# Optimization experiments

Hardware: AMD Instinct MI355X
Metric: run time of the kernel (lower is better)

The kernel has to match this reference:

```python
import jax, jax.numpy as jnp
import numpy as np

BATCH = 1024
SEQ = 80
VOCAB = 50000
EMB = 512
UNITS = 512


def setup_inputs() -> dict:
    key = jax.random.key(0)
    ks = jax.random.split(key, 10)
    s_in = 1.0 / np.sqrt(EMB)
    s_h = 1.0 / np.sqrt(UNITS)
    return {
        "inputs": jax.random.randint(ks[0], (BATCH, SEQ), 0, VOCAB, dtype=jnp.int64),
        "emb": jax.random.normal(ks[1], (VOCAB, EMB), dtype=jnp.float32) * 0.05,
        "W0x": jax.random.normal(ks[2], (EMB, UNITS), dtype=jnp.float32) * s_in,
        "W0h": jax.random.normal(ks[3], (UNITS, UNITS), dtype=jnp.float32) * s_h,
        "b0": jnp.zeros((UNITS,), dtype=jnp.float32),
        "W1x": jax.random.normal(ks[4], (UNITS, UNITS), dtype=jnp.float32) * s_h,
        "W1h": jax.random.normal(ks[5], (UNITS, UNITS), dtype=jnp.float32) * s_h,
        "b1": jnp.zeros((UNITS,), dtype=jnp.float32),
        "Wout": jax.random.normal(ks[6], (UNITS, 1), dtype=jnp.float32) * s_h,
        "bout": jnp.zeros((1,), dtype=jnp.float32),
    }


def reference(inputs, emb, W0x, W0h, b0, W1x, W1h, b1, Wout, bout):
    # Embedding lookup: [B, T, E]
    x = emb[inputs]
    # Time-major for scan: [T, B, E]
    xs = jnp.transpose(x, (1, 0, 2))

    h0 = jnp.zeros((inputs.shape[0], W0h.shape[0]), dtype=emb.dtype)
    h1 = jnp.zeros((inputs.shape[0], W1h.shape[0]), dtype=emb.dtype)

    def step(carry, x_t):
        h0, h1 = carry
        # SimpleRNNCell 0: tanh(x@Wx + h@Wh + b)  (dropout inactive at inference)
        h0 = jnp.tanh(x_t @ W0x + h0 @ W0h + b0)
        # SimpleRNNCell 1 stacked on cell 0's output
        h1 = jnp.tanh(h0 @ W1x + h1 @ W1h + b1)
        return (h0, h1), None

    (h0, h1), _ = jax.lax.scan(step, (h0, h1), xs)
    # Dense(1) on last-step hidden of layer 1, then sigmoid -> [B, 1]
    prob = jax.nn.sigmoid(h1 @ Wout + bout)
    return prob
```

## Files before the change

### kernel.cpp

```cpp
#include <hip/hip_runtime.h>
#include <hip/hip_bf16.h>
#include <math.h>

#define BATCH   1024
#define SEQ     80
#define EMB     512
#define UNITS   512
#define NBG     16
#define NJ      8
#define THREADS 512

#define H0_OFF (2u * 1024 * 1024)
#define H1_OFF (4u * 1024 * 1024)
#define FL_OFF (6u * 1024 * 1024)

typedef __attribute__((ext_vector_type(8))) short              bf16x8;
typedef __attribute__((ext_vector_type(8))) unsigned short     u16x8;
typedef __attribute__((ext_vector_type(4))) float              f32x4;
typedef __attribute__((ext_vector_type(2))) unsigned long long u64x2;

__device__ inline unsigned short f2bf(float f) {
    __hip_bfloat16 h = __float2bfloat16(f);
    return *reinterpret_cast<unsigned short*>(&h);
}
__device__ inline float bf2f(unsigned short u) {
    unsigned int x = ((unsigned int)u) << 16;
    return __uint_as_float(x);
}
__device__ inline float tanh_fast(float x) {
    float e = __expf(2.f * x);
    return 1.f - 2.f / (e + 1.f);
}
__device__ inline u16x8 pack8(float4 p0, float4 p1) {
    u16x8 v;
    v[0]=f2bf(p0.x); v[1]=f2bf(p0.y); v[2]=f2bf(p0.z); v[3]=f2bf(p0.w);
    v[4]=f2bf(p1.x); v[5]=f2bf(p1.y); v[6]=f2bf(p1.z); v[7]=f2bf(p1.w);
    return v;
}
__device__ inline void st_u16(unsigned short* p, unsigned short v) {
    __hip_atomic_store(p, v, __ATOMIC_RELAXED, __HIP_MEMORY_SCOPE_AGENT);
}
__device__ inline unsigned long long ld_u64(const unsigned long long* p) {
    return __hip_atomic_load(p, __ATOMIC_RELAXED, __HIP_MEMORY_SCOPE_AGENT);
}
__device__ inline int ld_flag(const int* p) {
    return __hip_atomic_load(p, __ATOMIC_RELAXED, __HIP_MEMORY_SCOPE_AGENT);
}

__global__ __launch_bounds__(256) void pack_weights(
    const float* __restrict__ W0x, const float* __restrict__ W0h,
    const float* __restrict__ W1x, const float* __restrict__ W1h,
    unsigned short* __restrict__ wpack)
{
    int g    = blockIdx.x * 4 + (threadIdx.x >> 6);
    int lane = threadIdx.x & 63;
    int type = g >> 10;
    int j    = (g >> 7) & 7;
    int mat  = (g >> 6) & 1;
    int kk   = (g >> 2) & 15;
    int nt   = g & 3;
    const float* M = type ? (mat ? W1h : W1x) : (mat ? W0h : W0x);
    int col  = j * 64 + nt * 16 + (lane & 15);
    int rowb = kk * 32 + (lane >> 4) * 8;

    u16x8 v;
#pragma unroll
    for (int jj = 0; jj < 8; ++jj)
        v[jj] = f2bf(M[(size_t)(rowb + jj) * UNITS + col]);
    *(u16x8*)(wpack + (size_t)g * 512 + lane * 8) = v;
}

#define WLD(mat, kk, nt)            ((((mat)*16 + (kk))*4 + (nt)) * 512)
#define RNG(slot, kkl, row, quad)   (((((slot)*2 + (kkl))*64 + (row))*4 + (quad)) * 8)

#define GATHER_GEMM(HB, PAR, MAT, A0, A1)                                      \
    do {                                                                       \
        const unsigned long long* hs_ = (const unsigned long long*)            \
            ((HB) + ((size_t)(PAR) * BATCH + rbase) * UNITS);                  \
        const int go_ = grow * 128 + gk8 * 2;                                  \
        u64x2 ld_[8];                                                          \
        _Pragma("unroll")                                                      \
        for (int s_ = 0; s_ < 3; ++s_) {                                       \
            ld_[s_][0] = ld_u64(hs_ + go_ + s_ * 16);                          \
            ld_[s_][1] = ld_u64(hs_ + go_ + s_ * 16 + 1);                      \
        }                                                                      \
        _Pragma("unroll")                                                      \
        for (int s_ = 0; s_ < 8; ++s_) {                                       \
            *(u64x2*)(ring + RNG(s_ & 1, gk8 >> 2, grow, gk8 & 3)) = ld_[s_];  \
            __syncthreads();                                                   \
            if (s_ + 3 < 8) {                                                  \
                ld_[s_+3][0] = ld_u64(hs_ + go_ + (s_+3) * 16);                \
                ld_[s_+3][1] = ld_u64(hs_ + go_ + (s_+3) * 16 + 1);            \
            }                                                                  \
            _Pragma("unroll")                                                  \
            for (int kl_ = 0; kl_ < 2; ++kl_) {                                \
                bf16x8 a_ = *(const bf16x8*)(ring + RNG(s_ & 1, kl_, arow, quad)); \
                int kg_ = s_ * 2 + kl_;                                        \
                A0 = __builtin_amdgcn_mfma_f32_16x16x32_bf16(a_,               \
                    *(const bf16x8*)(wlds + WLD(MAT, kg_, nt0) + lane*8), A0, 0,0,0); \
                A1 = __builtin_amdgcn_mfma_f32_16x16x32_bf16(a_,               \
                    *(const bf16x8*)(wlds + WLD(MAT, kg_, nt1) + lane*8), A1, 0,0,0); \
            }                                                                  \
        }                                                                      \
    } while (0)

#define XSTAGE_GEMM(TT, A0, A1)                                                \
    do {                                                                       \
        int t_   = (TT) < SEQ ? (TT) : SEQ - 1;                                \
        int idx_ = inputs[(rbase + grow) * SEQ + t_];                          \
        const float4* ep_ = (const float4*)(emb + (size_t)idx_ * EMB) + gk8*2; \
        float4 pa_[8], pb_[8];                                                 \
        _Pragma("unroll")                                                      \
        for (int s_ = 0; s_ < 3; ++s_) { pa_[s_] = ep_[s_*16]; pb_[s_] = ep_[s_*16+1]; } \
        _Pragma("unroll")                                                      \
        for (int s_ = 0; s_ < 8; ++s_) {                                       \
            *(u16x8*)(ring + RNG(s_ & 1, gk8 >> 2, grow, gk8 & 3)) =           \
                pack8(pa_[s_], pb_[s_]);                                       \
            __syncthreads();                                                   \
            if (s_ + 3 < 8) { pa_[s_+3] = ep_[(s_+3)*16]; pb_[s_+3] = ep_[(s_+3)*16+1]; } \
            _Pragma("unroll")                                                  \
            for (int kl_ = 0; kl_ < 2; ++kl_) {                                \
                bf16x8 a_ = *(const bf16x8*)(ring + RNG(s_ & 1, kl_, arow, quad)); \
                int kg_ = s_ * 2 + kl_;                                        \
                A0 = __builtin_amdgcn_mfma_f32_16x16x32_bf16(a_,               \
                    *(const bf16x8*)(wlds + WLD(0, kg_, nt0) + lane*8), A0, 0,0,0); \
                A1 = __builtin_amdgcn_mfma_f32_16x16x32_bf16(a_,               \
                    *(const bf16x8*)(wlds + WLD(0, kg_, nt1) + lane*8), A1, 0,0,0); \
            }                                                                  \
        }                                                                      \
    } while (0)

#define PUBLISH(HB, PAR, A0, A1)                                               \
    do {                                                                       \
        unsigned short* d_ = (HB) +                                            \
            ((size_t)(PAR) * BATCH + rbase + rg * 16 + quad * 4) * UNITS       \
            + c0 + l15;                                                        \
        _Pragma("unroll")                                                      \
        for (int i_ = 0; i_ < 4; ++i_) {                                       \
            st_u16(d_ + (size_t)i_ * UNITS + nt0 * 16, f2bf(tanh_fast(A0[i_]))); \
            st_u16(d_ + (size_t)i_ * UNITS + nt1 * 16, f2bf(tanh_fast(A1[i_]))); \
        }                                                                      \
    } while (0)

__global__ __launch_bounds__(THREADS, 1) void rnn_ls(
    const int*   __restrict__ inputs,
    const float* __restrict__ emb,
    const float* __restrict__ b0,
    const float* __restrict__ b1,
    const unsigned short* __restrict__ wpack,
    unsigned short* __restrict__ h0buf,
    unsigned short* __restrict__ h1buf,
    int* __restrict__ flag0,
    int* __restrict__ flag1,
    const float* __restrict__ Wout,
    const float* __restrict__ bout,
    float*       __restrict__ out)
{
    __shared__ __align__(16) unsigned short wlds[2 * 16 * 4 * 512];
    __shared__ __align__(16) unsigned short ring[2 * 2 * 64 * 4 * 8];

    const int tid   = threadIdx.x;
    const int w     = tid >> 6;
    const int lane  = tid & 63;
    const int quad  = lane >> 4;
    const int l15   = lane & 15;
    const int type  = blockIdx.x >> 7;
    const int bidx  = blockIdx.x & 127;
    const int bg    = bidx >> 3;
    const int j     = bidx & 7;
    const int rbase = bg * 64;
    const int c0    = j * 64;

    const int rg   = w >> 1;
    const int ntp  = w & 1;
    const int nt0  = 2 * ntp, nt1 = nt0 + 1;
    const int arow = rg * 16 + l15;
    const int grow = tid >> 3;
    const int gk8  = tid & 7;

    {
        const unsigned short* wsrc = wpack + (size_t)(type * 8 + j) * 128 * 512;
#pragma unroll
        for (int i = 0; i < 16; ++i)
            *(u16x8*)(wlds + (size_t)(i * 512 + tid) * 8) =
                *(const u16x8*)(wsrc + (size_t)(i * 512 + tid) * 8);
    }
    __syncthreads();

    const float* bp   = type ? b1 : b0;
    const float  bia0 = bp[c0 + nt0 * 16 + l15];
    const float  bia1 = bp[c0 + nt1 * 16 + l15];

    if (type == 0) {
        f32x4 aX0 = {bia0, bia0, bia0, bia0};
        f32x4 aX1 = {bia1, bia1, bia1, bia1};
        XSTAGE_GEMM(0, aX0, aX1);

        for (int r = 0; r < SEQ; ++r) {
            const int par = r & 1;
            if (tid < 8)
                while (ld_flag(flag0 + bg * 8 + tid) < r)
                    __builtin_amdgcn_s_sleep(1);
            else if (tid < 16)
                while (ld_flag(flag1 + bg * 8 + (tid - 8)) < r - 1)
                    __builtin_amdgcn_s_sleep(1);
            __asm__ volatile("" ::: "memory");
            __syncthreads();

            f32x4 a0 = aX0, a1 = aX1;
            GATHER_GEMM(h0buf, par ^ 1, 1, a0, a1);
            PUBLISH(h0buf, par, a0, a1);
            __syncthreads();
            if (tid == 0)
                __hip_atomic_store(flag0 + bg * 8 + j, r + 1,
                                   __ATOMIC_RELEASE, __HIP_MEMORY_SCOPE_AGENT);

            aX0 = (f32x4){bia0, bia0, bia0, bia0};
            aX1 = (f32x4){bia1, bia1, bia1, bia1};
            XSTAGE_GEMM(r + 1, aX0, aX1);
        }
    } else {
        for (int s = 0; s < SEQ; ++s) {
            const int par = s & 1;
            if (tid < 8)
                while (ld_flag(flag0 + bg * 8 + tid) < s + 1)
                    __builtin_amdgcn_s_sleep(1);
            else if (tid < 16)
                while (ld_flag(flag1 + bg * 8 + (tid - 8)) < s)
                    __builtin_amdgcn_s_sleep(1);
            __asm__ volatile("" ::: "memory");
            __syncthreads();

            f32x4 a0 = {bia0, bia0, bia0, bia0};
            f32x4 a1 = {bia1, bia1, bia1, bia1};
            GATHER_GEMM(h0buf, par,     0, a0, a1);
            GATHER_GEMM(h1buf, par ^ 1, 1, a0, a1);
            PUBLISH(h1buf, par, a0, a1);
            __syncthreads();
            if (tid == 0)
                __hip_atomic_store(flag1 + bg * 8 + j, s + 1,
                                   __ATOMIC_RELEASE, __HIP_MEMORY_SCOPE_AGENT);
        }

        if (j == 0) {
            if (tid < 8)
                while (ld_flag(flag1 + bg * 8 + tid) < SEQ)
                    __builtin_amdgcn_s_sleep(1);
            __asm__ volatile("" ::: "memory");
            __syncthreads();
            const unsigned long long* hs = (const unsigned long long*)
                (h1buf + ((size_t)((SEQ - 1) & 1) * BATCH + rbase) * UNITS);
#pragma unroll
            for (int i = 0; i < 8; ++i) {
                int row = w * 8 + i;
                unsigned long long q0 = ld_u64(hs + row * 128 + lane * 2);
                unsigned long long q1 = ld_u64(hs + row * 128 + lane * 2 + 1);
                u64x2 qq; qq[0] = q0; qq[1] = q1;
                u16x8 hv = *(u16x8*)&qq;
                float sacc = 0.f;
#pragma unroll
                for (int k = 0; k < 8; ++k)
                    sacc += bf2f(hv[k]) * Wout[lane * 8 + k];
#pragma unroll
                for (int off = 32; off > 0; off >>= 1)
                    sacc += __shfl_down(sacc, off);
                if (lane == 0) {
                    float z = sacc + bout[0];
                    out[rbase + row] = 1.f / (1.f + __expf(-z));
                }
            }
        }
    }
}

extern "C" void kernel_launch(void* const* d_in, const int* in_sizes, int n_in,
                              void* d_out, int out_size, void* d_ws, size_t ws_size,
                              hipStream_t stream) {
    const int*   inputs = (const int*)d_in[0];
    const float* emb    = (const float*)d_in[1];
    const float* W0x    = (const float*)d_in[2];
    const float* W0h    = (const float*)d_in[3];
    const float* b0     = (const float*)d_in[4];
    const float* W1x    = (const float*)d_in[5];
    const float* W1h    = (const float*)d_in[6];
    const float* b1     = (const float*)d_in[7];
    const float* Wout   = (const float*)d_in[8];
    const float* bout   = (const float*)d_in[9];
    float*       out    = (float*)d_out;

    unsigned short* wpack = (unsigned short*)d_ws;
    unsigned short* h0buf = (unsigned short*)((char*)d_ws + H0_OFF);
    unsigned short* h1buf = (unsigned short*)((char*)d_ws + H1_OFF);
    int* flag0 = (int*)((char*)d_ws + FL_OFF);
    int* flag1 = flag0 + 128;

    hipMemsetAsync((char*)d_ws + FL_OFF, 0, 1024, stream);
    hipMemsetAsync((char*)h0buf + (size_t)BATCH * UNITS * 2, 0,
                   (size_t)BATCH * UNITS * 2, stream);
    hipMemsetAsync((char*)h1buf + (size_t)BATCH * UNITS * 2, 0,
                   (size_t)BATCH * UNITS * 2, stream);
    pack_weights<<<512, 256, 0, stream>>>(W0x, W0h, W1x, W1h, wpack);
    rnn_ls<<<256, THREADS, 0, stream>>>(
        inputs, emb, b0, b1, wpack, h0buf, h1buf, flag0, flag1,
        Wout, bout, out);
}
```

Measured before the change: 1.277 ms.

## Load RNN activations directly into registers instead of staging through LDS ring

Replaces the cooperative LDS ring buffer (with per-slice __syncthreads) for hidden-state and embedding tiles with per-lane direct global loads of MFMA A-fragments into registers, then runs all 16 k-steps back to back. This removes the many barriers and LDS round trips inside every recurrent step. In exchange each wave loads its own rows redundantly and holds up to 32 bf16x8 fragments in registers. Launch bounds are also changed to allow two blocks per CU, which tightens the register budget.

```diff
diff --git a/kernel.cpp b/kernel.cpp
--- a/kernel.cpp
+++ b/kernel.cpp
@@ -70,64 +70,48 @@
     *(u16x8*)(wpack + (size_t)g * 512 + lane * 8) = v;
 }
 
-#define WLD(mat, kk, nt)            ((((mat)*16 + (kk))*4 + (nt)) * 512)
-#define RNG(slot, kkl, row, quad)   (((((slot)*2 + (kkl))*64 + (row))*4 + (quad)) * 8)
-
-#define GATHER_GEMM(HB, PAR, MAT, A0, A1)                                      \
+#define WLD(mat, kk, nt)  ((((mat)*16 + (kk))*4 + (nt)) * 512)
+
+#define GATHER_REG(AV, HB, PAR)                                                \
     do {                                                                       \
         const unsigned long long* hs_ = (const unsigned long long*)            \
-            ((HB) + ((size_t)(PAR) * BATCH + rbase) * UNITS);                  \
-        const int go_ = grow * 128 + gk8 * 2;                                  \
-        u64x2 ld_[8];                                                          \
-        _Pragma("unroll")                                                      \
-        for (int s_ = 0; s_ < 3; ++s_) {                                       \
-            ld_[s_][0] = ld_u64(hs_ + go_ + s_ * 16);                          \
-            ld_[s_][1] = ld_u64(hs_ + go_ + s_ * 16 + 1);                      \
-        }                                                                      \
-        _Pragma("unroll")                                                      \
-        for (int s_ = 0; s_ < 8; ++s_) {                                       \
-            *(u64x2*)(ring + RNG(s_ & 1, gk8 >> 2, grow, gk8 & 3)) = ld_[s_];  \
-            __syncthreads();                                                   \
-            if (s_ + 3 < 8) {                                                  \
-                ld_[s_+3][0] = ld_u64(hs_ + go_ + (s_+3) * 16);                \
-                ld_[s_+3][1] = ld_u64(hs_ + go_ + (s_+3) * 16 + 1);            \
-            }                                                                  \
-            _Pragma("unroll")                                                  \
-            for (int kl_ = 0; kl_ < 2; ++kl_) {                                \
-                bf16x8 a_ = *(const bf16x8*)(ring + RNG(s_ & 1, kl_, arow, quad)); \
-                int kg_ = s_ * 2 + kl_;                                        \
-                A0 = __builtin_amdgcn_mfma_f32_16x16x32_bf16(a_,               \
-                    *(const bf16x8*)(wlds + WLD(MAT, kg_, nt0) + lane*8), A0, 0,0,0); \
-                A1 = __builtin_amdgcn_mfma_f32_16x16x32_bf16(a_,               \
-                    *(const bf16x8*)(wlds + WLD(MAT, kg_, nt1) + lane*8), A1, 0,0,0); \
-            }                                                                  \
-        }                                                                      \
-    } while (0)
-
-#define XSTAGE_GEMM(TT, A0, A1)                                                \
+            ((HB) + ((size_t)(PAR) * BATCH + rbase + arow) * UNITS);           \
+        _Pragma("unroll")                                                      \
+        for (int ks_ = 0; ks_ < 16; ++ks_) {                                   \
+            u64x2 q_;                                                          \
+            q_[0] = ld_u64(hs_ + ks_ * 8 + quad * 2);                          \
+            q_[1] = ld_u64(hs_ + ks_ * 8 + quad * 2 + 1);                      \
+            (AV)[ks_] = *(bf16x8*)&q_;                                         \
+        }                                                                      \
+    } while (0)
+
+#define GEMM_LDS(AV, MAT, A0, A1)                                              \
+    do {                                                                       \
+        _Pragma("unroll")                                                      \
+        for (int kg_ = 0; kg_ < 16; ++kg_) {                                   \
+            bf16x8 b0_ = *(const bf16x8*)(wlds + WLD(MAT, kg_, nt0) + lane*8); \
+            bf16x8 b1_ = *(const bf16x8*)(wlds + WLD(MAT, kg_, nt1) + lane*8); \
+            A0 = __builtin_amdgcn_mfma_f32_16x16x32_bf16((AV)[kg_], b0_, A0,   \
+                                                         0, 0, 0);             \
+            A1 = __builtin_amdgcn_mfma_f32_16x16x32_bf16((AV)[kg_], b1_, A1,   \
+                                                         0, 0, 0);             \
+        }                                                                      \
+    } while (0)
+
+#define XSTAGE_REG(TT, A0, A1)                                                 \
     do {                                                                       \
         int t_   = (TT) < SEQ ? (TT) : SEQ - 1;                                \
-        int idx_ = inputs[(rbase + grow) * SEQ + t_];                          \
-        const float4* ep_ = (const float4*)(emb + (size_t)idx_ * EMB) + gk8*2; \
-        float4 pa_[8], pb_[8];                                                 \
-        _Pragma("unroll")                                                      \
-        for (int s_ = 0; s_ < 3; ++s_) { pa_[s_] = ep_[s_*16]; pb_[s_] = ep_[s_*16+1]; } \
-        _Pragma("unroll")                                                      \
-        for (int s_ = 0; s_ < 8; ++s_) {                                       \
-            *(u16x8*)(ring + RNG(s_ & 1, gk8 >> 2, grow, gk8 & 3)) =           \
-                pack8(pa_[s_], pb_[s_]);                                       \
-            __syncthreads();                                                   \
-            if (s_ + 3 < 8) { pa_[s_+3] = ep_[(s_+3)*16]; pb_[s_+3] = ep_[(s_+3)*16+1]; } \
-            _Pragma("unroll")                                                  \
-            for (int kl_ = 0; kl_ < 2; ++kl_) {                                \
-                bf16x8 a_ = *(const bf16x8*)(ring + RNG(s_ & 1, kl_, arow, quad)); \
-                int kg_ = s_ * 2 + kl_;                                        \
-                A0 = __builtin_amdgcn_mfma_f32_16x16x32_bf16(a_,               \
-                    *(const bf16x8*)(wlds + WLD(0, kg_, nt0) + lane*8), A0, 0,0,0); \
-                A1 = __builtin_amdgcn_mfma_f32_16x16x32_bf16(a_,               \
-                    *(const bf16x8*)(wlds + WLD(0, kg_, nt1) + lane*8), A1, 0,0,0); \
-            }                                                                  \
-        }                                                                      \
+        int idx_ = inputs[(rbase + arow) * SEQ + t_];                          \
+        const float4* ep_ = (const float4*)(emb + (size_t)idx_ * EMB);         \
+        bf16x8 xa_[16];                                                        \
+        _Pragma("unroll")                                                      \
+        for (int ks_ = 0; ks_ < 16; ++ks_) {                                   \
+            float4 pa_ = ep_[ks_ * 8 + quad * 2];                              \
+            float4 pb_ = ep_[ks_ * 8 + quad * 2 + 1];                          \
+            u16x8 vv_ = pack8(pa_, pb_);                                       \
+            xa_[ks_] = *(bf16x8*)&vv_;                                         \
+        }                                                                      \
+        GEMM_LDS(xa_, 0, A0, A1);                                              \
     } while (0)
 
 #define PUBLISH(HB, PAR, A0, A1)                                               \
@@ -142,7 +126,7 @@
         }                                                                      \
     } while (0)
 
-__global__ __launch_bounds__(THREADS, 1) void rnn_ls(
+__global__ __launch_bounds__(THREADS, 2) void rnn_lsr(
     const int*   __restrict__ inputs,
     const float* __restrict__ emb,
     const float* __restrict__ b0,
@@ -157,7 +141,6 @@
     float*       __restrict__ out)
 {
     __shared__ __align__(16) unsigned short wlds[2 * 16 * 4 * 512];
-    __shared__ __align__(16) unsigned short ring[2 * 2 * 64 * 4 * 8];
 
     const int tid   = threadIdx.x;
     const int w     = tid >> 6;
@@ -175,8 +158,6 @@
     const int ntp  = w & 1;
     const int nt0  = 2 * ntp, nt1 = nt0 + 1;
     const int arow = rg * 16 + l15;
-    const int grow = tid >> 3;
-    const int gk8  = tid & 7;
 
     {
         const unsigned short* wsrc = wpack + (size_t)(type * 8 + j) * 128 * 512;
@@ -194,7 +175,7 @@
     if (type == 0) {
         f32x4 aX0 = {bia0, bia0, bia0, bia0};
         f32x4 aX1 = {bia1, bia1, bia1, bia1};
-        XSTAGE_GEMM(0, aX0, aX1);
+        XSTAGE_REG(0, aX0, aX1);
 
         for (int r = 0; r < SEQ; ++r) {
             const int par = r & 1;
@@ -208,7 +189,9 @@
             __syncthreads();
 
             f32x4 a0 = aX0, a1 = aX1;
-            GATHER_GEMM(h0buf, par ^ 1, 1, a0, a1);
+            bf16x8 av[16];
+            GATHER_REG(av, h0buf, par ^ 1);
+            GEMM_LDS(av, 1, a0, a1);
             PUBLISH(h0buf, par, a0, a1);
             __syncthreads();
             if (tid == 0)
@@ -217,7 +200,7 @@
 
             aX0 = (f32x4){bia0, bia0, bia0, bia0};
             aX1 = (f32x4){bia1, bia1, bia1, bia1};
-            XSTAGE_GEMM(r + 1, aX0, aX1);
+            XSTAGE_REG(r + 1, aX0, aX1);
         }
     } else {
         for (int s = 0; s < SEQ; ++s) {
@@ -233,8 +216,11 @@
 
             f32x4 a0 = {bia0, bia0, bia0, bia0};
             f32x4 a1 = {bia1, bia1, bia1, bia1};
-            GATHER_GEMM(h0buf, par,     0, a0, a1);
-            GATHER_GEMM(h1buf, par ^ 1, 1, a0, a1);
+            bf16x8 av0[16], av1[16];
+            GATHER_REG(av0, h0buf, par);
+            GATHER_REG(av1, h1buf, par ^ 1);
+            GEMM_LDS(av0, 0, a0, a1);
+            GEMM_LDS(av1, 1, a0, a1);
             PUBLISH(h1buf, par, a0, a1);
             __syncthreads();
             if (tid == 0)
@@ -300,7 +286,7 @@
     hipMemsetAsync((char*)h1buf + (size_t)BATCH * UNITS * 2, 0,
                    (size_t)BATCH * UNITS * 2, stream);
     pack_weights<<<512, 256, 0, stream>>>(W0x, W0h, W1x, W1h, wpack);
-    rnn_ls<<<256, THREADS, 0, stream>>>(
+    rnn_lsr<<<256, THREADS, 0, stream>>>(
         inputs, emb, b0, b1, wpack, h0buf, h1buf, flag0, flag1,
         Wout, bout, out);
 }
```

After: 1.965 ms. +53.8%, slower.
